# Performance work log

Hardware: AMD Instinct MI355X
Metric: run time of the kernel (lower is better)

Reference implementation:

```python
import jax, jax.numpy as jnp
import numpy as np

B, MAXN, NVT, NINP, NHID, NHEAD, NL, NZ = 1024, 32, 16, 256, 512, 8, 6, 64
HID = MAXN * NHID
EPS = 1e-5
SCALE = 1.0 / np.sqrt(NHID // NHEAD)


def setup_inputs() -> dict:
    key = jax.random.key(0)
    ks = jax.random.split(key, 16)
    s = 0.02
    d = {}
    d["node_types"] = jax.random.randint(ks[0], (B, MAXN), 0, NVT, dtype=jnp.int32)
    d["adj_bits"] = jax.random.randint(ks[1], (B, MAXN, MAXN), 0, 2, dtype=jnp.int32)
    d["Wpos"] = jax.random.normal(ks[2], (MAXN, NINP), jnp.float32) * s
    d["bpos"] = jnp.zeros((NINP,), jnp.float32)
    d["Wnode"] = jax.random.normal(ks[3], (NVT, NINP), jnp.float32) * s
    d["bnode"] = jnp.zeros((NINP,), jnp.float32)
    for i, n in enumerate(["Wq", "Wk", "Wv", "Wo", "W1", "W2"]):
        d["enc_" + n] = jax.random.normal(ks[4 + i], (NL, NHID, NHID), jnp.float32) * s
    for n in ["bq", "bk", "bv", "bo", "b1", "b2"]:
        d["enc_" + n] = jnp.zeros((NL, NHID), jnp.float32)
    d["ln1_g"] = jnp.ones((NL, NHID), jnp.float32)
    d["ln1_b"] = jnp.zeros((NL, NHID), jnp.float32)
    d["ln2_g"] = jnp.ones((NL, NHID), jnp.float32)
    d["ln2_b"] = jnp.zeros((NL, NHID), jnp.float32)
    d["Wfc1"] = jax.random.normal(ks[10], (HID, NZ), jnp.float32) * s
    d["bfc1"] = jnp.zeros((NZ,), jnp.float32)
    d["Wfc2"] = jax.random.normal(ks[11], (HID, NZ), jnp.float32) * s
    d["bfc2"] = jnp.zeros((NZ,), jnp.float32)
    return d


def _ln(x, g, b):
    m = x.mean(-1, keepdims=True)
    v = ((x - m) ** 2).mean(-1, keepdims=True)
    return (x - m) * jax.lax.rsqrt(v + EPS) * g + b


def _dag_attn_bias(adj_bits):
    # _mask_generate: transitive closure via matmul powers; log-depth squaring
    # over a boolean semiring (min(.,1) after each add) gives identical reachability.
    iu = jnp.triu(jnp.ones((MAXN, MAXN), jnp.float32), 1)  # enforce DAG
    adj = adj_bits.astype(jnp.float32) * iu  # [B,N,N]
    reach = adj
    for _ in range(int(np.ceil(np.log2(MAXN)))):
        reach = jnp.minimum(reach + jnp.matmul(reach, reach), 1.0)
    # original: mask = (sum_powers + I) < 0.5 (True=disallowed), then transpose(1,2)
    allowed = (jnp.swapaxes(reach, 1, 2) + jnp.eye(MAXN, dtype=jnp.float32)) > 0.5
    return jnp.where(allowed, 0.0, -jnp.inf)[:, None, :, :]  # [B,1,N,N]


def _encode(node_types, adj_bits, Wpos, bpos, Wnode, bnode,
            enc_Wq, enc_bq, enc_Wk, enc_bk, enc_Wv, enc_bv, enc_Wo, enc_bo,
            ln1_g, ln1_b, enc_W1, enc_b1, enc_W2, enc_b2, ln2_g, ln2_b,
            Wfc1, bfc1, Wfc2, bfc2):
    node_feat = jax.nn.relu(Wnode[node_types] + bnode)               # [B,N,ninp]
    pos_feat = jnp.broadcast_to(Wpos + bpos, (B, MAXN, NINP))        # position = node index
    x = jnp.concatenate([node_feat, pos_feat], -1)                   # [B,N,512]
    bias = _dag_attn_bias(adj_bits)
    dh = NHID // NHEAD
    for l in range(NL):
        q = (x @ enc_Wq[l] + enc_bq[l]).reshape(B, MAXN, NHEAD, dh)
        k = (x @ enc_Wk[l] + enc_bk[l]).reshape(B, MAXN, NHEAD, dh)
        v = (x @ enc_Wv[l] + enc_bv[l]).reshape(B, MAXN, NHEAD, dh)
        s = jnp.einsum('bqhd,bkhd->bhqk', q, k) * SCALE + bias
        a = jax.nn.softmax(s, axis=-1)
        o = jnp.einsum('bhqk,bkhd->bqhd', a, v).reshape(B, MAXN, NHID)
        x = _ln(x + o @ enc_Wo[l] + enc_bo[l], ln1_g[l], ln1_b[l])    # post-LN
        f = jax.nn.relu(x @ enc_W1[l] + enc_b1[l]) @ enc_W2[l] + enc_b2[l]
        x = _ln(x + f, ln2_g[l], ln2_b[l])
    mem = x.reshape(B, HID)
    return mem @ Wfc1 + bfc1, mem @ Wfc2 + bfc2


def reference(node_types, adj_bits, Wpos, bpos, Wnode, bnode,
              enc_Wq, enc_bq, enc_Wk, enc_bk, enc_Wv, enc_bv, enc_Wo, enc_bo,
              ln1_g, ln1_b, enc_W1, enc_b1, enc_W2, enc_b2, ln2_g, ln2_b,
              Wfc1, bfc1, Wfc2, bfc2):
    return _encode(node_types, adj_bits, Wpos, bpos, Wnode, bnode,
                   enc_Wq, enc_bq, enc_Wk, enc_bk, enc_Wv, enc_bv, enc_Wo, enc_bo,
                   ln1_g, ln1_b, enc_W1, enc_b1, enc_W2, enc_b2, ln2_g, ln2_b,
                   Wfc1, bfc1, Wfc2, bfc2)
```

## Files before the change

### kernel.cpp

```cpp
#include <hip/hip_runtime.h>


typedef unsigned short u16;
typedef unsigned int u32;
typedef __attribute__((ext_vector_type(8))) short bf16x8;
typedef __attribute__((ext_vector_type(4))) float f32x4;

#define NB 1024
#define MAXN 32
#define NHID 512
#define NHEAD 8
#define NLAY 6
#define MTOT (NB * MAXN)
#define ATT_SCALE 0.125f
#define LN_EPS 1e-5f

__device__ __forceinline__ float bf2f(u16 h) { return __uint_as_float(((u32)h) << 16); }
__device__ __forceinline__ u16 f2bf(float f) {
  u32 u = __float_as_uint(f);
  return (u16)((u + 0x7fffu + ((u >> 16) & 1u)) >> 16);
}

__device__ __forceinline__ void gload16(const void* g, void* l) {
  __builtin_amdgcn_global_load_lds((const __attribute__((address_space(1))) void*)g,
                                   (__attribute__((address_space(3))) void*)l, 16, 0, 0);
}

__device__ __forceinline__ void xcd_remap(int l, int NX, int& mt, int& nt) {
  int xcd = l & 7;
  int s = l >> 3;
  int mg = s / NX;
  nt = s - mg * NX;
  mt = mg * 8 + xcd;
}

__global__ __launch_bounds__(256) void mask_k(const int* __restrict__ adj, u32* __restrict__ mask) {
  __shared__ u32 r[8][32];
  int tid = threadIdx.x;
  int g = tid >> 5, i = tid & 31;
  int b = blockIdx.x * 8 + g;
  const int* ab = adj + ((long)b * 32 + i) * 32;
  u32 m = 0;
  for (int j = i + 1; j < 32; ++j)
    if (ab[j]) m |= (1u << j);
  r[g][i] = m;
  __syncthreads();
  for (int it = 0; it < 5; ++it) {
    u32 cur = r[g][i];
    u32 acc = cur;
    #pragma unroll
    for (int j = 0; j < 32; ++j)
      if ((cur >> j) & 1u) acc |= r[g][j];
    __syncthreads();
    r[g][i] = acc;
    __syncthreads();
  }
  u32 am = 1u << i;
  #pragma unroll
  for (int k = 0; k < 32; ++k) am |= ((r[g][k] >> i) & 1u) << k;
  mask[b * 32 + i] = am;
}

__global__ __launch_bounds__(256) void embed_k(const int* __restrict__ types,
    const float* __restrict__ Wpos, const float* __restrict__ bpos,
    const float* __restrict__ Wnode, const float* __restrict__ bnode,
    u16* __restrict__ xb) {
  int i = blockIdx.x * 256 + threadIdx.x;
  int row = i >> 7, c = (i & 127) * 4;
  int b = row >> 5, n = row & 31;
  float v[4];
  if (c < 256) {
    int tp = types[b * 32 + n];
    const float* w = &Wnode[tp * 256 + c];
    #pragma unroll
    for (int j = 0; j < 4; ++j) v[j] = fmaxf(w[j] + bnode[c + j], 0.f);
  } else {
    int cc = c - 256;
    const float* w = &Wpos[n * 256 + cc];
    #pragma unroll
    for (int j = 0; j < 4; ++j) v[j] = w[j] + bpos[cc + j];
  }
  ushort4 h; h.x = f2bf(v[0]); h.y = f2bf(v[1]); h.z = f2bf(v[2]); h.w = f2bf(v[3]);
  *(ushort4*)&xb[(long)row * NHID + c] = h;
}

__global__ __launch_bounds__(256) void tconv_k(const float* __restrict__ W,
    u16* __restrict__ Wt, int n_off, int n_total) {
  __shared__ float tile[32][33];
  int l = blockIdx.z;
  int k0 = blockIdx.x * 32, n0 = blockIdx.y * 32;
  int tx = threadIdx.x & 31, ty = threadIdx.x >> 5;
  const float* src = W + (size_t)l * NHID * NHID;
  #pragma unroll
  for (int i = 0; i < 4; ++i)
    tile[ty + 8 * i][tx] = src[(size_t)(k0 + ty + 8 * i) * NHID + n0 + tx];
  __syncthreads();
  u16* dst = Wt + (size_t)l * n_total * NHID;
  #pragma unroll
  for (int i = 0; i < 4; ++i)
    dst[(size_t)(n_off + n0 + ty + 8 * i) * NHID + k0 + tx] = f2bf(tile[tx][ty + 8 * i]);
}

__global__ __launch_bounds__(256, 2) void gemm_qkv(
    const u16* __restrict__ A, const u16* __restrict__ Bt,
    const float* __restrict__ bq, const float* __restrict__ bk,
    const float* __restrict__ bv, u16* __restrict__ qk, u16* __restrict__ v) {
  __shared__ u16 As[3][128 * 32];
  __shared__ u16 Bs[3][256 * 32];
  const int tid = threadIdx.x;
  const int wave = tid >> 6, lane = tid & 63;
  int mt, nt_;
  xcd_remap(blockIdx.x + gridDim.x * blockIdx.y, gridDim.x, mt, nt_);
  const long m0 = (long)mt * 128;
  const int n0 = nt_ * 256;
  const int wr = wave >> 1, wc = wave & 1;
  const int srow = lane >> 2;
  const int sg = (lane & 3) ^ ((srow >> 1) & 3);
  const int fr = lane & 15;
  const int kq = lane >> 4;
  f32x4 acc[4][8] = {};

  auto stage = [&](int buf, int k0) {
    #pragma unroll
    for (int i = 0; i < 2; ++i) {
      int c = 2 * wave + i;
      gload16(A + (m0 + 16 * c + srow) * 512L + k0 + sg * 8, &As[buf][c * 512]);
    }
    #pragma unroll
    for (int i = 0; i < 4; ++i) {
      int c = 4 * wave + i;
      gload16(Bt + (long)(n0 + 16 * c + srow) * 512 + k0 + sg * 8, &Bs[buf][c * 512]);
    }
  };
  stage(0, 0);
  stage(1, 32);
  const int kqx = (kq ^ ((fr >> 1) & 3)) * 8;
  int cs = 0;
  #pragma unroll 1
  for (int t = 0; t < 16; ++t) {
    if (t + 1 < 16) asm volatile("s_waitcnt vmcnt(6)" ::: "memory");
    else            asm volatile("s_waitcnt vmcnt(0)" ::: "memory");
    __builtin_amdgcn_s_barrier();
    if (t + 2 < 16) {
      int nb = cs + 2; if (nb >= 3) nb -= 3;
      stage(nb, (t + 2) * 32);
    }
    const u16* Asl = As[cs];
    const u16* Bsl = Bs[cs];
    bf16x8 af[4], bfv[8];
    #pragma unroll
    for (int mi = 0; mi < 4; ++mi)
      af[mi] = *(const bf16x8*)&Asl[(wr * 64 + mi * 16 + fr) * 32 + kqx];
    #pragma unroll
    for (int ni = 0; ni < 8; ++ni)
      bfv[ni] = *(const bf16x8*)&Bsl[(wc * 128 + ni * 16 + fr) * 32 + kqx];
    #pragma unroll
    for (int mi = 0; mi < 4; ++mi)
      #pragma unroll
      for (int ni = 0; ni < 8; ++ni)
        acc[mi][ni] = __builtin_amdgcn_mfma_f32_16x16x32_bf16(bfv[ni], af[mi], acc[mi][ni], 0, 0, 0);
    if (++cs == 3) cs = 0;
  }

  #pragma unroll
  for (int mi = 0; mi < 4; ++mi) {
    long r = m0 + wr * 64 + mi * 16 + fr;
    #pragma unroll
    for (int ni = 0; ni < 8; ++ni) {
      int n = n0 + wc * 128 + ni * 16 + kq * 4;
      const float* bp = (n < 512) ? bq : ((n < 1024) ? bk : bv);
      float4 bvv = *(const float4*)&bp[n & 511];
      ushort4 st;
      st.x = f2bf(acc[mi][ni][0] + bvv.x);
      st.y = f2bf(acc[mi][ni][1] + bvv.y);
      st.z = f2bf(acc[mi][ni][2] + bvv.z);
      st.w = f2bf(acc[mi][ni][3] + bvv.w);
      if (n < 1024) *(ushort4*)&qk[r * 1024 + n] = st;
      else          *(ushort4*)&v[r * 512 + (n - 1024)] = st;
    }
  }
}

__global__ __launch_bounds__(256, 2) void gemm_relu(
    const u16* __restrict__ A, const u16* __restrict__ Bt,
    const float* __restrict__ bias0, u16* __restrict__ Cout) {
  __shared__ u16 As[3][128 * 32];
  __shared__ u16 Bs[3][256 * 32];
  const int tid = threadIdx.x;
  const int wave = tid >> 6, lane = tid & 63;
  int mt, nt_;
  xcd_remap(blockIdx.x + gridDim.x * blockIdx.y, gridDim.x, mt, nt_);
  const long m0 = (long)mt * 128;
  const int n0 = nt_ * 256;
  const int wr = wave >> 1, wc = wave & 1;
  const int srow = lane >> 2;
  const int sg = (lane & 3) ^ ((srow >> 1) & 3);
  const int fr = lane & 15;
  const int kq = lane >> 4;
  f32x4 acc[4][8] = {};

  auto stage = [&](int buf, int k0) {
    #pragma unroll
    for (int i = 0; i < 2; ++i) {
      int c = 2 * wave + i;
      gload16(A + (m0 + 16 * c + srow) * 512L + k0 + sg * 8, &As[buf][c * 512]);
    }
    #pragma unroll
    for (int i = 0; i < 4; ++i) {
      int c = 4 * wave + i;
      gload16(Bt + (long)(n0 + 16 * c + srow) * 512 + k0 + sg * 8, &Bs[buf][c * 512]);
    }
  };
  stage(0, 0);
  stage(1, 32);
  const int kqx = (kq ^ ((fr >> 1) & 3)) * 8;
  int cs = 0;
  #pragma unroll 1
  for (int t = 0; t < 16; ++t) {
    if (t + 1 < 16) asm volatile("s_waitcnt vmcnt(6)" ::: "memory");
    else            asm volatile("s_waitcnt vmcnt(0)" ::: "memory");
    __builtin_amdgcn_s_barrier();
    if (t + 2 < 16) {
      int nb = cs + 2; if (nb >= 3) nb -= 3;
      stage(nb, (t + 2) * 32);
    }
    const u16* Asl = As[cs];
    const u16* Bsl = Bs[cs];
    bf16x8 af[4], bfv[8];
    #pragma unroll
    for (int mi = 0; mi < 4; ++mi)
      af[mi] = *(const bf16x8*)&Asl[(wr * 64 + mi * 16 + fr) * 32 + kqx];
    #pragma unroll
    for (int ni = 0; ni < 8; ++ni)
      bfv[ni] = *(const bf16x8*)&Bsl[(wc * 128 + ni * 16 + fr) * 32 + kqx];
    #pragma unroll
    for (int mi = 0; mi < 4; ++mi)
      #pragma unroll
      for (int ni = 0; ni < 8; ++ni)
        acc[mi][ni] = __builtin_amdgcn_mfma_f32_16x16x32_bf16(bfv[ni], af[mi], acc[mi][ni], 0, 0, 0);
    if (++cs == 3) cs = 0;
  }

  #pragma unroll
  for (int mi = 0; mi < 4; ++mi) {
    long r = m0 + wr * 64 + mi * 16 + fr;
    #pragma unroll
    for (int ni = 0; ni < 8; ++ni) {
      int n = n0 + wc * 128 + ni * 16 + kq * 4;
      float4 bvv = *(const float4*)&bias0[n];
      ushort4 st;
      st.x = f2bf(fmaxf(acc[mi][ni][0] + bvv.x, 0.f));
      st.y = f2bf(fmaxf(acc[mi][ni][1] + bvv.y, 0.f));
      st.z = f2bf(fmaxf(acc[mi][ni][2] + bvv.z, 0.f));
      st.w = f2bf(fmaxf(acc[mi][ni][3] + bvv.w, 0.f));
      *(ushort4*)&Cout[r * 512 + n] = st;
    }
  }
}

__global__ __launch_bounds__(512, 1) void gemm_ln(
    const u16* __restrict__ A, const u16* __restrict__ Bt,
    const float* __restrict__ bias0, const float* __restrict__ g,
    const float* __restrict__ b, u16* __restrict__ xb) {
  __shared__ u16 As[3][128 * 32];
  __shared__ u16 Bs[3][512 * 32];
  __shared__ float red[2][64][4][2];
  const int tid = threadIdx.x;
  const int wave = tid >> 6, lane = tid & 63;
  const long m0 = (long)blockIdx.x * 128;
  const int wr = wave >> 2, wc = wave & 3;
  const int srow = lane >> 2;
  const int sg = (lane & 3) ^ ((srow >> 1) & 3);
  const int fr = lane & 15;
  const int kq = lane >> 4;
  f32x4 acc[4][8] = {};

  auto stage = [&](int buf, int k0) {
    gload16(A + (m0 + 16 * wave + srow) * 512L + k0 + sg * 8, &As[buf][wave * 512]);
    #pragma unroll
    for (int i = 0; i < 4; ++i) {
      int c = 4 * wave + i;
      gload16(Bt + (long)(16 * c + srow) * 512 + k0 + sg * 8, &Bs[buf][c * 512]);
    }
  };
  stage(0, 0);
  stage(1, 32);
  const int kqx = (kq ^ ((fr >> 1) & 3)) * 8;
  int cs = 0;
  #pragma unroll 1
  for (int t = 0; t < 16; ++t) {
    if (t + 1 < 16) asm volatile("s_waitcnt vmcnt(5)" ::: "memory");
    else            asm volatile("s_waitcnt vmcnt(0)" ::: "memory");
    __builtin_amdgcn_s_barrier();
    if (t + 2 < 16) {
      int nb = cs + 2; if (nb >= 3) nb -= 3;
      stage(nb, (t + 2) * 32);
    }
    const u16* Asl = As[cs];
    const u16* Bsl = Bs[cs];
    bf16x8 af[4], bfv[8];
    #pragma unroll
    for (int mi = 0; mi < 4; ++mi)
      af[mi] = *(const bf16x8*)&Asl[(wr * 64 + mi * 16 + fr) * 32 + kqx];
    #pragma unroll
    for (int ni = 0; ni < 8; ++ni)
      bfv[ni] = *(const bf16x8*)&Bsl[(wc * 128 + ni * 16 + fr) * 32 + kqx];
    #pragma unroll
    for (int mi = 0; mi < 4; ++mi)
      #pragma unroll
      for (int ni = 0; ni < 8; ++ni)
        acc[mi][ni] = __builtin_amdgcn_mfma_f32_16x16x32_bf16(bfv[ni], af[mi], acc[mi][ni], 0, 0, 0);
    if (++cs == 3) cs = 0;
  }

  float s[4], sq[4];
  #pragma unroll
  for (int mi = 0; mi < 4; ++mi) {
    long r = m0 + wr * 64 + mi * 16 + fr;
    float ss = 0.f, qq = 0.f;
    #pragma unroll
    for (int ni = 0; ni < 8; ++ni) {
      int n = wc * 128 + ni * 16 + kq * 4;
      float4 bvv = *(const float4*)&bias0[n];
      ushort4 rv = *(const ushort4*)&xb[r * 512 + n];
      float y0 = acc[mi][ni][0] + bvv.x + bf2f(rv.x);
      float y1 = acc[mi][ni][1] + bvv.y + bf2f(rv.y);
      float y2 = acc[mi][ni][2] + bvv.z + bf2f(rv.z);
      float y3 = acc[mi][ni][3] + bvv.w + bf2f(rv.w);
      acc[mi][ni][0] = y0; acc[mi][ni][1] = y1;
      acc[mi][ni][2] = y2; acc[mi][ni][3] = y3;
      ss += y0 + y1 + y2 + y3;
      qq += y0 * y0 + y1 * y1 + y2 * y2 + y3 * y3;
    }
    s[mi] = ss; sq[mi] = qq;
  }
  #pragma unroll
  for (int mi = 0; mi < 4; ++mi) {
    s[mi] += __shfl_xor(s[mi], 16);  sq[mi] += __shfl_xor(sq[mi], 16);
    s[mi] += __shfl_xor(s[mi], 32);  sq[mi] += __shfl_xor(sq[mi], 32);
  }
  if (lane < 16) {
    #pragma unroll
    for (int mi = 0; mi < 4; ++mi) {
      red[wr][mi * 16 + fr][wc][0] = s[mi];
      red[wr][mi * 16 + fr][wc][1] = sq[mi];
    }
  }
  __syncthreads();
  #pragma unroll
  for (int mi = 0; mi < 4; ++mi) {
    int rl = mi * 16 + fr;
    float S = red[wr][rl][0][0] + red[wr][rl][1][0] + red[wr][rl][2][0] + red[wr][rl][3][0];
    float Q = red[wr][rl][0][1] + red[wr][rl][1][1] + red[wr][rl][2][1] + red[wr][rl][3][1];
    float mean = S * (1.f / 512.f);
    float inv = rsqrtf(Q * (1.f / 512.f) - mean * mean + LN_EPS);
    long r = m0 + wr * 64 + rl;
    #pragma unroll
    for (int ni = 0; ni < 8; ++ni) {
      int n = wc * 128 + ni * 16 + kq * 4;
      float4 g4 = *(const float4*)&g[n];
      float4 b4 = *(const float4*)&b[n];
      ushort4 st;
      st.x = f2bf((acc[mi][ni][0] - mean) * inv * g4.x + b4.x);
      st.y = f2bf((acc[mi][ni][1] - mean) * inv * g4.y + b4.y);
      st.z = f2bf((acc[mi][ni][2] - mean) * inv * g4.z + b4.z);
      st.w = f2bf((acc[mi][ni][3] - mean) * inv * g4.w + b4.w);
      *(ushort4*)&xb[r * 512 + n] = st;
    }
  }
}

__global__ __launch_bounds__(256) void attn_k(const u16* __restrict__ qk,
    const u16* __restrict__ vfull, const u32* __restrict__ mask, u16* __restrict__ o) {
  __shared__ u16 vs_[4][64][40];
  __shared__ u16 p_lds[4][32][40];
  int tid = threadIdx.x;
  int w = tid >> 6, lane = tid & 63;
  int idx = blockIdx.x * 4 + w;
  int b = idx >> 3, h = idx & 7;
  const u16* qbase = qk + (long)b * 32 * 1024 + h * 64;
  const u16* kbase = qbase + 512;
  int g = lane >> 4, r = lane & 15;

  int node = lane >> 1, dh = lane & 1;
  const u16* vsrc = vfull + ((long)b * 32 + node) * 512 + h * 64 + dh * 32;
  bf16x8 vr[4];
  #pragma unroll
  for (int i = 0; i < 4; ++i) vr[i] = *(const bf16x8*)(vsrc + i * 8);

  f32x4 s[2][2] = {};
  #pragma unroll
  for (int ks = 0; ks < 2; ++ks) {
    bf16x8 kf[2], qf[2];
    #pragma unroll
    for (int mi = 0; mi < 2; ++mi)
      kf[mi] = *(const bf16x8*)(kbase + (long)(mi * 16 + r) * 1024 + ks * 32 + g * 8);
    #pragma unroll
    for (int nj = 0; nj < 2; ++nj)
      qf[nj] = *(const bf16x8*)(qbase + (long)(nj * 16 + r) * 1024 + ks * 32 + g * 8);
    #pragma unroll
    for (int mi = 0; mi < 2; ++mi)
      #pragma unroll
      for (int nj = 0; nj < 2; ++nj)
        s[mi][nj] = __builtin_amdgcn_mfma_f32_16x16x32_bf16(kf[mi], qf[nj], s[mi][nj], 0, 0, 0);
  }

  #pragma unroll
  for (int i = 0; i < 4; ++i)
    #pragma unroll
    for (int t = 0; t < 8; ++t)
      vs_[w][dh * 32 + i * 8 + t][node] = (u16)vr[i][t];

  #pragma unroll
  for (int nj = 0; nj < 2; ++nj) {
    int q = nj * 16 + r;
    u32 mk = mask[b * 32 + q];
    float vv[8];
    float mx = -1e30f;
    #pragma unroll
    for (int mi = 0; mi < 2; ++mi)
      #pragma unroll
      for (int j = 0; j < 4; ++j) {
        int k = mi * 16 + g * 4 + j;
        float val = ((mk >> k) & 1u) ? s[mi][nj][j] * ATT_SCALE : -1e30f;
        vv[mi * 4 + j] = val;
        mx = fmaxf(mx, val);
      }
    mx = fmaxf(mx, __shfl_xor(mx, 16));
    mx = fmaxf(mx, __shfl_xor(mx, 32));
    float sum = 0.f;
    #pragma unroll
    for (int i = 0; i < 8; ++i) { vv[i] = __expf(vv[i] - mx); sum += vv[i]; }
    sum += __shfl_xor(sum, 16);
    sum += __shfl_xor(sum, 32);
    float inv = 1.f / sum;
    #pragma unroll
    for (int mi = 0; mi < 2; ++mi) {
      ushort4 pk;
      pk.x = f2bf(vv[mi * 4 + 0] * inv);
      pk.y = f2bf(vv[mi * 4 + 1] * inv);
      pk.z = f2bf(vv[mi * 4 + 2] * inv);
      pk.w = f2bf(vv[mi * 4 + 3] * inv);
      *(ushort4*)&p_lds[w][q][mi * 16 + g * 4] = pk;
    }
  }

  bf16x8 pa[2];
  #pragma unroll
  for (int mi = 0; mi < 2; ++mi)
    pa[mi] = *(const bf16x8*)&p_lds[w][mi * 16 + r][g * 8];
  f32x4 oacc[2][4] = {};
  #pragma unroll
  for (int nd = 0; nd < 4; ++nd) {
    bf16x8 vf = *(const bf16x8*)&vs_[w][nd * 16 + r][g * 8];
    #pragma unroll
    for (int mi = 0; mi < 2; ++mi)
      oacc[mi][nd] = __builtin_amdgcn_mfma_f32_16x16x32_bf16(pa[mi], vf, oacc[mi][nd], 0, 0, 0);
  }
  #pragma unroll
  for (int mi = 0; mi < 2; ++mi)
    #pragma unroll
    for (int j = 0; j < 4; ++j) {
      int q = mi * 16 + g * 4 + j;
      u16* og = o + ((long)b * 32 + q) * NHID + h * 64;
      #pragma unroll
      for (int nd = 0; nd < 4; ++nd)
        og[nd * 16 + r] = f2bf(oacc[mi][nd][j]);
    }
}

__global__ __launch_bounds__(256) void fcT_k(const float* __restrict__ W1,
    const float* __restrict__ W2, u16* __restrict__ Wt) {
  __shared__ float t[64][65];
  int sel = blockIdx.y;
  const float* W = sel ? W2 : W1;
  int k0 = blockIdx.x * 64;
  int tx = threadIdx.x & 63, ty = threadIdx.x >> 6;
  #pragma unroll
  for (int i = 0; i < 16; ++i)
    t[ty + 4 * i][tx] = W[(long)(k0 + ty + 4 * i) * 64 + tx];
  __syncthreads();
  #pragma unroll
  for (int i = 0; i < 16; ++i)
    Wt[(long)(sel * 64 + ty + 4 * i) * 16384 + k0 + tx] = f2bf(t[tx][ty + 4 * i]);
}

__global__ __launch_bounds__(256, 2) void gemm_fc(const u16* __restrict__ A,
    const u16* __restrict__ Bt, float* __restrict__ part) {
  __shared__ u16 As[3][128 * 32];
  __shared__ u16 Bs[3][128 * 32];
  const int tid = threadIdx.x;
  const int wave = tid >> 6, lane = tid & 63;
  const int ks = blockIdx.x;
  const long m0 = (long)blockIdx.y * 128;
  const int kbase = ks * 512;
  const int wr = wave >> 1, wc = wave & 1;
  const int srow = lane >> 2;
  const int sg = (lane & 3) ^ ((srow >> 1) & 3);
  const int fr = lane & 15;
  const int kq = lane >> 4;
  f32x4 acc[4][4] = {};
  auto stage = [&](int buf, int k0) {
    #pragma unroll
    for (int i = 0; i < 2; ++i) {
      int c = 2 * wave + i;
      gload16(A + (m0 + 16 * c + srow) * 16384L + kbase + k0 + sg * 8, &As[buf][c * 512]);
      gload16(Bt + (long)(16 * c + srow) * 16384L + kbase + k0 + sg * 8, &Bs[buf][c * 512]);
    }
  };
  stage(0, 0);
  stage(1, 32);
  const int kqx = (kq ^ ((fr >> 1) & 3)) * 8;
  int cs = 0;
  #pragma unroll 1
  for (int t = 0; t < 16; ++t) {
    if (t + 1 < 16) asm volatile("s_waitcnt vmcnt(4)" ::: "memory");
    else            asm volatile("s_waitcnt vmcnt(0)" ::: "memory");
    __builtin_amdgcn_s_barrier();
    if (t + 2 < 16) {
      int nb = cs + 2; if (nb >= 3) nb -= 3;
      stage(nb, (t + 2) * 32);
    }
    const u16* Asl = As[cs];
    const u16* Bsl = Bs[cs];
    bf16x8 af[4], bfv[4];
    #pragma unroll
    for (int mi = 0; mi < 4; ++mi)
      af[mi] = *(const bf16x8*)&Asl[(wr * 64 + mi * 16 + fr) * 32 + kqx];
    #pragma unroll
    for (int ni = 0; ni < 4; ++ni)
      bfv[ni] = *(const bf16x8*)&Bsl[(wc * 64 + ni * 16 + fr) * 32 + kqx];
    #pragma unroll
    for (int mi = 0; mi < 4; ++mi)
      #pragma unroll
      for (int ni = 0; ni < 4; ++ni)
        acc[mi][ni] = __builtin_amdgcn_mfma_f32_16x16x32_bf16(bfv[ni], af[mi], acc[mi][ni], 0, 0, 0);
    if (++cs == 3) cs = 0;
  }
  #pragma unroll
  for (int mi = 0; mi < 4; ++mi) {
    long rr = m0 + wr * 64 + mi * 16 + fr;
    #pragma unroll
    for (int ni = 0; ni < 4; ++ni) {
      int n = wc * 64 + ni * 16 + kq * 4;
      *(float4*)&part[((long)ks * 1024 + rr) * 128 + n] =
          make_float4(acc[mi][ni][0], acc[mi][ni][1], acc[mi][ni][2], acc[mi][ni][3]);
    }
  }
}

__global__ __launch_bounds__(256) void fc_red_k(const float* __restrict__ part,
    const float* __restrict__ bfc1, const float* __restrict__ bfc2,
    float* __restrict__ out) {
  int idx = blockIdx.x * 256 + threadIdx.x;
  int sel = idx >> 16;
  int rem = idx & 65535;
  int b = rem >> 6, z = rem & 63;
  float v = sel ? bfc2[z] : bfc1[z];
  #pragma unroll
  for (int ks = 0; ks < 32; ++ks)
    v += part[((long)ks * 1024 + b) * 128 + sel * 64 + z];
  out[idx] = v;
}

extern "C" void kernel_launch(void* const* d_in, const int* in_sizes, int n_in,
                              void* d_out, int out_size, void* d_ws, size_t ws_size,
                              hipStream_t stream) {
  const int* node_types = (const int*)d_in[0];
  const int* adj_bits = (const int*)d_in[1];
  const float* Wpos = (const float*)d_in[2];
  const float* bpos = (const float*)d_in[3];
  const float* Wnode = (const float*)d_in[4];
  const float* bnode = (const float*)d_in[5];
  const float* eWq = (const float*)d_in[6];
  const float* eWk = (const float*)d_in[7];
  const float* eWv = (const float*)d_in[8];
  const float* eWo = (const float*)d_in[9];
  const float* eW1 = (const float*)d_in[10];
  const float* eW2 = (const float*)d_in[11];
  const float* ebq = (const float*)d_in[12];
  const float* ebk = (const float*)d_in[13];
  const float* ebv = (const float*)d_in[14];
  const float* ebo = (const float*)d_in[15];
  const float* eb1 = (const float*)d_in[16];
  const float* eb2 = (const float*)d_in[17];
  const float* ln1g = (const float*)d_in[18];
  const float* ln1b = (const float*)d_in[19];
  const float* ln2g = (const float*)d_in[20];
  const float* ln2b = (const float*)d_in[21];
  const float* Wfc1 = (const float*)d_in[22];
  const float* bfc1 = (const float*)d_in[23];
  const float* Wfc2 = (const float*)d_in[24];
  const float* bfc2 = (const float*)d_in[25];

  char* ws = (char*)d_ws;
  size_t off = 0;
  auto carve = [&](size_t bytes) {
    void* p = ws + off;
    off += (bytes + 255) & ~(size_t)255;
    return p;
  };
  u16* Wqkv_t = (u16*)carve((size_t)NLAY * 1536 * 512 * 2);
  u16* Wo_t = (u16*)carve((size_t)NLAY * 512 * 512 * 2);
  u16* W1_t = (u16*)carve((size_t)NLAY * 512 * 512 * 2);
  u16* W2_t = (u16*)carve((size_t)NLAY * 512 * 512 * 2);
  u16* xb = (u16*)carve((size_t)MTOT * NHID * 2);
  u16* qk = (u16*)carve((size_t)MTOT * 1024 * 2);
  u16* vbuf = (u16*)carve((size_t)MTOT * NHID * 2);
  u16* obuf = (u16*)carve((size_t)MTOT * NHID * 2);
  u32* maskb = (u32*)carve((size_t)NB * MAXN * 4);
  u16* hbuf = obuf;
  u16* Wt_fc = qk;
  float* part_fc = (float*)obuf;

  mask_k<<<NB / 8, 256, 0, stream>>>(adj_bits, maskb);
  embed_k<<<(MTOT * 128) / 256, 256, 0, stream>>>(node_types, Wpos, bpos, Wnode, bnode, xb);
  dim3 tg(16, 16, NLAY);
  tconv_k<<<tg, 256, 0, stream>>>(eWq, Wqkv_t, 0, 1536);
  tconv_k<<<tg, 256, 0, stream>>>(eWk, Wqkv_t, 512, 1536);
  tconv_k<<<tg, 256, 0, stream>>>(eWv, Wqkv_t, 1024, 1536);
  tconv_k<<<tg, 256, 0, stream>>>(eWo, Wo_t, 0, 512);
  tconv_k<<<tg, 256, 0, stream>>>(eW1, W1_t, 0, 512);
  tconv_k<<<tg, 256, 0, stream>>>(eW2, W2_t, 0, 512);

  for (int l = 0; l < NLAY; ++l) {
    size_t lw = (size_t)l * 512 * 512;
    gemm_qkv<<<dim3(6, MTOT / 128), 256, 0, stream>>>(
        xb, Wqkv_t + (size_t)l * 1536 * 512,
        ebq + l * 512, ebk + l * 512, ebv + l * 512, qk, vbuf);
    attn_k<<<NB * NHEAD / 4, 256, 0, stream>>>(qk, vbuf, maskb, obuf);
    gemm_ln<<<MTOT / 128, 512, 0, stream>>>(
        obuf, Wo_t + lw, ebo + l * 512, ln1g + l * 512, ln1b + l * 512, xb);
    gemm_relu<<<dim3(2, MTOT / 128), 256, 0, stream>>>(
        xb, W1_t + lw, eb1 + l * 512, hbuf);
    gemm_ln<<<MTOT / 128, 512, 0, stream>>>(
        hbuf, W2_t + lw, eb2 + l * 512, ln2g + l * 512, ln2b + l * 512, xb);
  }

  fcT_k<<<dim3(256, 2), 256, 0, stream>>>(Wfc1, Wfc2, Wt_fc);
  gemm_fc<<<dim3(32, 8), 256, 0, stream>>>(xb, Wt_fc, part_fc);
  fc_red_k<<<512, 256, 0, stream>>>(part_fc, bfc1, bfc2, (float*)d_out);
}
```

Baseline: 1.361 ms.

## Shrink GEMM tiles to 128x128 with double buffering and higher occupancy

The QKV, FFN1 and FC GEMMs move from 128x256 tiles with a three-stage LDS pipeline to 128x128 tiles with two-stage double buffering, and launch bounds are raised so four blocks can share a CU. The FFN1 GEMM becomes a templated gemm_bt with generic N/K and optional ReLU or residual epilogues. s_setprio is placed around the MFMA sections of all GEMMs, including gemm_ln. The aim is more resident waves to hide latency and more blocks for better load balance. In exchange there is less reuse per tile, more global traffic, and a shallower prefetch with a full vmcnt(0) wait on every iteration.

```diff
diff --git a/kernel.cpp b/kernel.cpp
--- a/kernel.cpp
+++ b/kernel.cpp
@@ -101,73 +101,64 @@
     dst[(size_t)(n_off + n0 + ty + 8 * i) * NHID + k0 + tx] = f2bf(tile[tx][ty + 8 * i]);
 }
 
-__global__ __launch_bounds__(256, 2) void gemm_qkv(
+__global__ __launch_bounds__(256, 4) void gemm_qkv(
     const u16* __restrict__ A, const u16* __restrict__ Bt,
     const float* __restrict__ bq, const float* __restrict__ bk,
     const float* __restrict__ bv, u16* __restrict__ qk, u16* __restrict__ v) {
-  __shared__ u16 As[3][128 * 32];
-  __shared__ u16 Bs[3][256 * 32];
+  __shared__ u16 As[2][128 * 32];
+  __shared__ u16 Bs[2][128 * 32];
   const int tid = threadIdx.x;
   const int wave = tid >> 6, lane = tid & 63;
   int mt, nt_;
   xcd_remap(blockIdx.x + gridDim.x * blockIdx.y, gridDim.x, mt, nt_);
   const long m0 = (long)mt * 128;
-  const int n0 = nt_ * 256;
+  const int n0 = nt_ * 128;
   const int wr = wave >> 1, wc = wave & 1;
   const int srow = lane >> 2;
   const int sg = (lane & 3) ^ ((srow >> 1) & 3);
   const int fr = lane & 15;
   const int kq = lane >> 4;
-  f32x4 acc[4][8] = {};
+  f32x4 acc[4][4] = {};
 
   auto stage = [&](int buf, int k0) {
     #pragma unroll
     for (int i = 0; i < 2; ++i) {
       int c = 2 * wave + i;
       gload16(A + (m0 + 16 * c + srow) * 512L + k0 + sg * 8, &As[buf][c * 512]);
-    }
-    #pragma unroll
-    for (int i = 0; i < 4; ++i) {
-      int c = 4 * wave + i;
       gload16(Bt + (long)(n0 + 16 * c + srow) * 512 + k0 + sg * 8, &Bs[buf][c * 512]);
     }
   };
   stage(0, 0);
-  stage(1, 32);
   const int kqx = (kq ^ ((fr >> 1) & 3)) * 8;
-  int cs = 0;
   #pragma unroll 1
   for (int t = 0; t < 16; ++t) {
-    if (t + 1 < 16) asm volatile("s_waitcnt vmcnt(6)" ::: "memory");
-    else            asm volatile("s_waitcnt vmcnt(0)" ::: "memory");
+    asm volatile("s_waitcnt vmcnt(0)" ::: "memory");
     __builtin_amdgcn_s_barrier();
-    if (t + 2 < 16) {
-      int nb = cs + 2; if (nb >= 3) nb -= 3;
-      stage(nb, (t + 2) * 32);
-    }
-    const u16* Asl = As[cs];
-    const u16* Bsl = Bs[cs];
-    bf16x8 af[4], bfv[8];
+    if (t + 1 < 16) stage((t + 1) & 1, (t + 1) * 32);
+    const u16* Asl = As[t & 1];
+    const u16* Bsl = Bs[t & 1];
+    __builtin_amdgcn_s_setprio(1);
+    bf16x8 af[4], bfv[4];
     #pragma unroll
     for (int mi = 0; mi < 4; ++mi)
       af[mi] = *(const bf16x8*)&Asl[(wr * 64 + mi * 16 + fr) * 32 + kqx];
     #pragma unroll
-    for (int ni = 0; ni < 8; ++ni)
-      bfv[ni] = *(const bf16x8*)&Bsl[(wc * 128 + ni * 16 + fr) * 32 + kqx];
+    for (int ni = 0; ni < 4; ++ni)
+      bfv[ni] = *(const bf16x8*)&Bsl[(wc * 64 + ni * 16 + fr) * 32 + kqx];
     #pragma unroll
     for (int mi = 0; mi < 4; ++mi)
       #pragma unroll
-      for (int ni = 0; ni < 8; ++ni)
+      for (int ni = 0; ni < 4; ++ni)
         acc[mi][ni] = __builtin_amdgcn_mfma_f32_16x16x32_bf16(bfv[ni], af[mi], acc[mi][ni], 0, 0, 0);
-    if (++cs == 3) cs = 0;
+    __builtin_amdgcn_s_setprio(0);
   }
 
   #pragma unroll
   for (int mi = 0; mi < 4; ++mi) {
     long r = m0 + wr * 64 + mi * 16 + fr;
     #pragma unroll
-    for (int ni = 0; ni < 8; ++ni) {
-      int n = n0 + wc * 128 + ni * 16 + kq * 4;
+    for (int ni = 0; ni < 4; ++ni) {
+      int n = n0 + wc * 64 + ni * 16 + kq * 4;
       const float* bp = (n < 512) ? bq : ((n < 1024) ? bk : bv);
       float4 bvv = *(const float4*)&bp[n & 511];
       ushort4 st;
@@ -181,79 +172,82 @@
   }
 }
 
-__global__ __launch_bounds__(256, 2) void gemm_relu(
+template <int EPI>
+__global__ __launch_bounds__(256, 4) void gemm_bt(
     const u16* __restrict__ A, const u16* __restrict__ Bt,
-    const float* __restrict__ bias0, u16* __restrict__ Cout) {
-  __shared__ u16 As[3][128 * 32];
-  __shared__ u16 Bs[3][256 * 32];
+    const float* __restrict__ bias0, const u16* __restrict__ res,
+    u16* __restrict__ Cout, int N, int K) {
+  __shared__ u16 As[2][128 * 32];
+  __shared__ u16 Bs[2][128 * 32];
   const int tid = threadIdx.x;
   const int wave = tid >> 6, lane = tid & 63;
   int mt, nt_;
   xcd_remap(blockIdx.x + gridDim.x * blockIdx.y, gridDim.x, mt, nt_);
   const long m0 = (long)mt * 128;
-  const int n0 = nt_ * 256;
+  const int n0 = nt_ * 128;
   const int wr = wave >> 1, wc = wave & 1;
   const int srow = lane >> 2;
   const int sg = (lane & 3) ^ ((srow >> 1) & 3);
   const int fr = lane & 15;
   const int kq = lane >> 4;
-  f32x4 acc[4][8] = {};
+  f32x4 acc[4][4] = {};
 
   auto stage = [&](int buf, int k0) {
     #pragma unroll
     for (int i = 0; i < 2; ++i) {
       int c = 2 * wave + i;
-      gload16(A + (m0 + 16 * c + srow) * 512L + k0 + sg * 8, &As[buf][c * 512]);
-    }
-    #pragma unroll
-    for (int i = 0; i < 4; ++i) {
-      int c = 4 * wave + i;
-      gload16(Bt + (long)(n0 + 16 * c + srow) * 512 + k0 + sg * 8, &Bs[buf][c * 512]);
+      gload16(A + (m0 + 16 * c + srow) * (long)K + k0 + sg * 8, &As[buf][c * 512]);
+      gload16(Bt + (long)(n0 + 16 * c + srow) * K + k0 + sg * 8, &Bs[buf][c * 512]);
     }
   };
   stage(0, 0);
-  stage(1, 32);
+  const int nt = K >> 5;
   const int kqx = (kq ^ ((fr >> 1) & 3)) * 8;
-  int cs = 0;
   #pragma unroll 1
-  for (int t = 0; t < 16; ++t) {
-    if (t + 1 < 16) asm volatile("s_waitcnt vmcnt(6)" ::: "memory");
-    else            asm volatile("s_waitcnt vmcnt(0)" ::: "memory");
+  for (int t = 0; t < nt; ++t) {
+    asm volatile("s_waitcnt vmcnt(0)" ::: "memory");
     __builtin_amdgcn_s_barrier();
-    if (t + 2 < 16) {
-      int nb = cs + 2; if (nb >= 3) nb -= 3;
-      stage(nb, (t + 2) * 32);
-    }
-    const u16* Asl = As[cs];
-    const u16* Bsl = Bs[cs];
-    bf16x8 af[4], bfv[8];
+    if (t + 1 < nt) stage((t + 1) & 1, (t + 1) * 32);
+    const u16* Asl = As[t & 1];
+    const u16* Bsl = Bs[t & 1];
+    __builtin_amdgcn_s_setprio(1);
+    bf16x8 af[4], bfv[4];
     #pragma unroll
     for (int mi = 0; mi < 4; ++mi)
       af[mi] = *(const bf16x8*)&Asl[(wr * 64 + mi * 16 + fr) * 32 + kqx];
     #pragma unroll
-    for (int ni = 0; ni < 8; ++ni)
-      bfv[ni] = *(const bf16x8*)&Bsl[(wc * 128 + ni * 16 + fr) * 32 + kqx];
+    for (int ni = 0; ni < 4; ++ni)
+      bfv[ni] = *(const bf16x8*)&Bsl[(wc * 64 + ni * 16 + fr) * 32 + kqx];
     #pragma unroll
     for (int mi = 0; mi < 4; ++mi)
       #pragma unroll
-      for (int ni = 0; ni < 8; ++ni)
+      for (int ni = 0; ni < 4; ++ni)
         acc[mi][ni] = __builtin_amdgcn_mfma_f32_16x16x32_bf16(bfv[ni], af[mi], acc[mi][ni], 0, 0, 0);
-    if (++cs == 3) cs = 0;
+    __builtin_amdgcn_s_setprio(0);
   }
 
   #pragma unroll
   for (int mi = 0; mi < 4; ++mi) {
     long r = m0 + wr * 64 + mi * 16 + fr;
     #pragma unroll
-    for (int ni = 0; ni < 8; ++ni) {
-      int n = n0 + wc * 128 + ni * 16 + kq * 4;
+    for (int ni = 0; ni < 4; ++ni) {
+      int n = n0 + wc * 64 + ni * 16 + kq * 4;
       float4 bvv = *(const float4*)&bias0[n];
+      float v0 = acc[mi][ni][0] + bvv.x;
+      float v1 = acc[mi][ni][1] + bvv.y;
+      float v2 = acc[mi][ni][2] + bvv.z;
+      float v3 = acc[mi][ni][3] + bvv.w;
+      if (EPI == 2) {
+        v0 = fmaxf(v0, 0.f); v1 = fmaxf(v1, 0.f);
+        v2 = fmaxf(v2, 0.f); v3 = fmaxf(v3, 0.f);
+      }
+      if (EPI == 3) {
+        ushort4 rv = *(const ushort4*)&res[r * (long)N + n];
+        v0 += bf2f(rv.x); v1 += bf2f(rv.y); v2 += bf2f(rv.z); v3 += bf2f(rv.w);
+      }
       ushort4 st;
-      st.x = f2bf(fmaxf(acc[mi][ni][0] + bvv.x, 0.f));
-      st.y = f2bf(fmaxf(acc[mi][ni][1] + bvv.y, 0.f));
-      st.z = f2bf(fmaxf(acc[mi][ni][2] + bvv.z, 0.f));
-      st.w = f2bf(fmaxf(acc[mi][ni][3] + bvv.w, 0.f));
-      *(ushort4*)&Cout[r * 512 + n] = st;
+      st.x = f2bf(v0); st.y = f2bf(v1); st.z = f2bf(v2); st.w = f2bf(v3);
+      *(ushort4*)&Cout[r * (long)N + n] = st;
     }
   }
 }
@@ -298,6 +292,7 @@
     }
     const u16* Asl = As[cs];
     const u16* Bsl = Bs[cs];
+    __builtin_amdgcn_s_setprio(1);
     bf16x8 af[4], bfv[8];
     #pragma unroll
     for (int mi = 0; mi < 4; ++mi)
@@ -310,6 +305,7 @@
       #pragma unroll
       for (int ni = 0; ni < 8; ++ni)
         acc[mi][ni] = __builtin_amdgcn_mfma_f32_16x16x32_bf16(bfv[ni], af[mi], acc[mi][ni], 0, 0, 0);
+    __builtin_amdgcn_s_setprio(0);
     if (++cs == 3) cs = 0;
   }
 
@@ -485,10 +481,10 @@
     Wt[(long)(sel * 64 + ty + 4 * i) * 16384 + k0 + tx] = f2bf(t[tx][ty + 4 * i]);
 }
 
-__global__ __launch_bounds__(256, 2) void gemm_fc(const u16* __restrict__ A,
+__global__ __launch_bounds__(256, 4) void gemm_fc(const u16* __restrict__ A,
     const u16* __restrict__ Bt, float* __restrict__ part) {
-  __shared__ u16 As[3][128 * 32];
-  __shared__ u16 Bs[3][128 * 32];
+  __shared__ u16 As[2][128 * 32];
+  __shared__ u16 Bs[2][128 * 32];
   const int tid = threadIdx.x;
   const int wave = tid >> 6, lane = tid & 63;
   const int ks = blockIdx.x;
@@ -509,20 +505,15 @@
     }
   };
   stage(0, 0);
-  stage(1, 32);
   const int kqx = (kq ^ ((fr >> 1) & 3)) * 8;
-  int cs = 0;
   #pragma unroll 1
   for (int t = 0; t < 16; ++t) {
-    if (t + 1 < 16) asm volatile("s_waitcnt vmcnt(4)" ::: "memory");
-    else            asm volatile("s_waitcnt vmcnt(0)" ::: "memory");
+    asm volatile("s_waitcnt vmcnt(0)" ::: "memory");
     __builtin_amdgcn_s_barrier();
-    if (t + 2 < 16) {
-      int nb = cs + 2; if (nb >= 3) nb -= 3;
-      stage(nb, (t + 2) * 32);
-    }
-    const u16* Asl = As[cs];
-    const u16* Bsl = Bs[cs];
+    if (t + 1 < 16) stage((t + 1) & 1, (t + 1) * 32);
+    const u16* Asl = As[t & 1];
+    const u16* Bsl = Bs[t & 1];
+    __builtin_amdgcn_s_setprio(1);
     bf16x8 af[4], bfv[4];
     #pragma unroll
     for (int mi = 0; mi < 4; ++mi)
@@ -535,7 +526,7 @@
       #pragma unroll
       for (int ni = 0; ni < 4; ++ni)
         acc[mi][ni] = __builtin_amdgcn_mfma_f32_16x16x32_bf16(bfv[ni], af[mi], acc[mi][ni], 0, 0, 0);
-    if (++cs == 3) cs = 0;
+    __builtin_amdgcn_s_setprio(0);
   }
   #pragma unroll
   for (int mi = 0; mi < 4; ++mi) {
@@ -625,14 +616,14 @@
 
   for (int l = 0; l < NLAY; ++l) {
     size_t lw = (size_t)l * 512 * 512;
-    gemm_qkv<<<dim3(6, MTOT / 128), 256, 0, stream>>>(
+    gemm_qkv<<<dim3(12, MTOT / 128), 256, 0, stream>>>(
         xb, Wqkv_t + (size_t)l * 1536 * 512,
         ebq + l * 512, ebk + l * 512, ebv + l * 512, qk, vbuf);
     attn_k<<<NB * NHEAD / 4, 256, 0, stream>>>(qk, vbuf, maskb, obuf);
     gemm_ln<<<MTOT / 128, 512, 0, stream>>>(
         obuf, Wo_t + lw, ebo + l * 512, ln1g + l * 512, ln1b + l * 512, xb);
-    gemm_relu<<<dim3(2, MTOT / 128), 256, 0, stream>>>(
-        xb, W1_t + lw, eb1 + l * 512, hbuf);
+    gemm_bt<2><<<dim3(4, MTOT / 128), 256, 0, stream>>>(
+        xb, W1_t + lw, eb1 + l * 512, nullptr, hbuf, 512, 512);
     gemm_ln<<<MTOT / 128, 512, 0, stream>>>(
         hbuf, W2_t + lw, eb2 + l * 512, ln2g + l * 512, ln2b + l * 512, xb);
   }
```

Measured after the change: 1.340 ms. About the same (-1.5%).
